# Performance work log

Hardware: AMD Instinct MI355X
Metric: run time of the kernel (lower is better)

## Reference

```python
import jax, jax.numpy as jnp
import numpy as np

B, T, D_IN, D_OUT = 4, 2048, 1024, 1024


def setup_inputs() -> dict:
    key = jax.random.key(0)
    k1, k2, k3, k4 = jax.random.split(key, 4)
    x = jax.random.normal(k1, (B, T, D_IN), dtype=jnp.float32)
    W_q = jax.random.normal(k2, (D_OUT, D_IN), dtype=jnp.float32) * 0.02
    W_k = jax.random.normal(k3, (D_OUT, D_IN), dtype=jnp.float32) * 0.02
    W_v = jax.random.normal(k4, (D_OUT, D_IN), dtype=jnp.float32) * 0.02
    return {"x": x, "W_q": W_q, "W_k": W_k, "W_v": W_v}


def reference(x, W_q, W_k, W_v):
    b, t, d_in = x.shape
    d_out = W_q.shape[0]
    # Linear projections (torch Linear: y = x @ W.T), no bias
    q = jnp.einsum("btd,od->bto", x, W_q)
    k = jnp.einsum("btd,od->bto", x, W_k)
    v = jnp.einsum("btd,od->bto", x, W_v)
    # Raw scores [b, t, t]
    scores = jnp.einsum("bqd,bkd->bqk", q, k)
    # Faithful to the source: tril with diagonal=1 => position i sees j <= i+1
    mask = jnp.tril(jnp.ones((t, t), dtype=bool), k=1)
    scores = jnp.where(mask, scores, -jnp.inf)
    # Scale by sqrt(d_out) (full d_out, single head), stable softmax
    attn = jax.nn.softmax(scores / jnp.sqrt(jnp.asarray(d_out, x.dtype)), axis=-1)
    # dropout=0.0 -> identity
    return jnp.einsum("bqk,bkd->bqd", attn, v)
```

## Files before the change

kernel.cpp:

```cpp
#include <hip/hip_runtime.h>
#include <hip/hip_bf16.h>

typedef unsigned short u16;
typedef __attribute__((ext_vector_type(8))) short short8v;
typedef __attribute__((ext_vector_type(4))) float float4v;

__device__ inline u16 f2b(float f) {
  __hip_bfloat16 h = __float2bfloat16(f);
  union { __hip_bfloat16 h; u16 s; } u;
  u.h = h;
  return u.s;
}

__device__ inline float b2f(u16 s) {
  union { u16 s[2]; float f; } u;
  u.s[0] = 0; u.s[1] = s;
  return u.f;
}

__device__ inline void gload_lds16(const u16* g, u16* l) {
  __builtin_amdgcn_global_load_lds(
      (const __attribute__((address_space(1))) void*)g,
      (__attribute__((address_space(3))) void*)l, 16, 0, 0);
}

__global__ __launch_bounds__(256) void cvt_f32_bf16(const float* __restrict__ in,
                                                    u16* __restrict__ out, int n4) {
  for (int i = blockIdx.x * blockDim.x + threadIdx.x; i < n4;
       i += gridDim.x * blockDim.x) {
    float4 v = ((const float4*)in)[i];
    ushort4 o;
    o.x = f2b(v.x); o.y = f2b(v.y); o.z = f2b(v.z); o.w = f2b(v.w);
    ((ushort4*)out)[i] = o;
  }
}

template <int MODE, typename CT>
__global__ __launch_bounds__(256, 2)
void gemm6(const u16* __restrict__ A, int lda, long sA,
           const u16* __restrict__ B, int ldb, long sB,
           CT* __restrict__ C, int ldc, long sC, int K) {
  constexpr int BM = 128, BN = 128;
  constexpr int A_U16 = BM * 64;
  constexpr int TILE_U16 = (BM + BN) * 64;
  constexpr int TILE_BYTES = TILE_U16 * 2;
  __shared__ __align__(16) u16 lds[2 * TILE_U16];

  const int z = blockIdx.z;
  A += (long)z * sA;
  B += (long)z * sB;

  int bx = blockIdx.x;
  if (MODE == 2) bx = gridDim.x - 1 - bx;
  const int m0 = bx * BM;
  const int n0 = blockIdx.y * BN;
  if (MODE == 1 && n0 > m0 + BM) return;
  int Keff = K;
  if (MODE == 2) Keff = min(m0 + BM + 1, K);
  const int nk = (Keff + 63) >> 6;

  const int tid  = threadIdx.x;
  const int lane = tid & 63;
  const int wid  = tid >> 6;
  const int wr   = wid >> 1;
  const int wc   = wid & 1;

  const u16* gsrc[8];
  int loff[8];
#pragma unroll
  for (int j = 0; j < 4; ++j) {
    int c = tid + j * 256;
    int r = c >> 3;
    int kg = ((c & 7) ^ (r & 7)) * 8;
    gsrc[j] = A + (long)(m0 + r) * lda + kg;
    loff[j] = c * 8;
  }
#pragma unroll
  for (int j = 0; j < 4; ++j) {
    int c = tid + j * 256;
    int r = c >> 3;
    int kg = ((c & 7) ^ (r & 7)) * 8;
    gsrc[4 + j] = B + (long)(n0 + r) * ldb + kg;
    loff[4 + j] = A_U16 + c * 8;
  }

#define STAGE_ALL(T_, DST_)                                                 \
  {                                                                         \
    _Pragma("unroll")                                                       \
    for (int s = 0; s < 8; ++s)                                             \
      gload_lds16(gsrc[s] + (long)(T_) * 64, (DST_) + loff[s]);             \
  }

  const int kl  = (lane >> 4) * 16;
  const int swz = (lane & 7) << 4;
  const int kx0 = kl ^ swz;
  const int kx1 = (64 + kl) ^ swz;
  const int abase = (wr * 64 + (lane & 15)) * 128;
  const int bbase = 2 * A_U16 + (wc * 64 + (lane & 15)) * 128;

  float4v acc[4][4];
#pragma unroll
  for (int i = 0; i < 4; ++i)
#pragma unroll
    for (int j = 0; j < 4; ++j)
      acc[i][j] = (float4v){0.f, 0.f, 0.f, 0.f};

  STAGE_ALL(0, lds);
  asm volatile("s_waitcnt vmcnt(0)" ::: "memory");
  __builtin_amdgcn_s_barrier();

  for (int t = 0; t < nk; ++t) {
    const char* bb = (const char*)lds + (t & 1) * TILE_BYTES;
    u16* sb = lds + ((t & 1) ^ 1) * TILE_U16;

    short8v a0[4], b0[4], a1[4], b1[4];
#pragma unroll
    for (int mi = 0; mi < 4; ++mi) {
      a0[mi] = *(const short8v*)(bb + abase + mi * 2048 + kx0);
      a1[mi] = *(const short8v*)(bb + abase + mi * 2048 + kx1);
    }
#pragma unroll
    for (int ni = 0; ni < 4; ++ni) {
      b0[ni] = *(const short8v*)(bb + bbase + ni * 2048 + kx0);
      b1[ni] = *(const short8v*)(bb + bbase + ni * 2048 + kx1);
    }
    if (t + 1 < nk) STAGE_ALL(t + 1, sb);

    asm volatile("s_waitcnt lgkmcnt(0)" ::: "memory");
    __builtin_amdgcn_sched_barrier(0);
    __builtin_amdgcn_s_setprio(1);
#pragma unroll
    for (int mi = 0; mi < 4; ++mi)
#pragma unroll
      for (int ni = 0; ni < 4; ++ni)
        acc[mi][ni] = __builtin_amdgcn_mfma_f32_16x16x32_bf16(
            a0[mi], b0[ni], acc[mi][ni], 0, 0, 0);
#pragma unroll
    for (int mi = 0; mi < 4; ++mi)
#pragma unroll
      for (int ni = 0; ni < 4; ++ni)
        acc[mi][ni] = __builtin_amdgcn_mfma_f32_16x16x32_bf16(
            a1[mi], b1[ni], acc[mi][ni], 0, 0, 0);
    __builtin_amdgcn_s_setprio(0);

    asm volatile("s_waitcnt vmcnt(0)" ::: "memory");
    __builtin_amdgcn_s_barrier();
  }
#undef STAGE_ALL

  CT* c = C + (long)z * sC;
  const int r0base = m0 + wr * 64 + ((lane >> 4) << 2);
  const int cbase  = n0 + wc * 64 + (lane & 15);
#pragma unroll
  for (int mi = 0; mi < 4; ++mi) {
#pragma unroll
    for (int ni = 0; ni < 4; ++ni) {
      const int r0 = r0base + mi * 16;
      const int cc = cbase + ni * 16;
#pragma unroll
      for (int r = 0; r < 4; ++r) {
        float v = acc[mi][ni][r];
        if constexpr (__is_same(CT, float)) c[(long)(r0 + r) * ldc + cc] = v;
        else                                c[(long)(r0 + r) * ldc + cc] = f2b(v);
      }
    }
  }
}

__global__ __launch_bounds__(256)
void softmax_kernel(u16* __restrict__ SP, int T) {
  const int  i    = blockIdx.x & (T - 1);
  const long base = (long)blockIdx.x * T;
  const int  nvis = min(i + 2, T);
  const int  capJ = min(T, ((i >> 7) << 7) + 192);
  const float scale = 0.03125f;

  __shared__ float red[4];

  const int j0 = threadIdx.x * 8;
  float v[8];
  float m = -INFINITY;
  if (j0 < nvis) {
    short8v raw = *(const short8v*)&SP[base + j0];
#pragma unroll
    for (int e = 0; e < 8; ++e) {
      float f = (j0 + e < nvis) ? b2f((u16)raw[e]) * scale : -INFINITY;
      v[e] = f;
      m = fmaxf(m, f);
    }
  }
#pragma unroll
  for (int o = 32; o; o >>= 1) m = fmaxf(m, __shfl_xor(m, o));
  const int wid = threadIdx.x >> 6;
  if ((threadIdx.x & 63) == 0) red[wid] = m;
  __syncthreads();
  m = fmaxf(fmaxf(red[0], red[1]), fmaxf(red[2], red[3]));
  __syncthreads();

  float s = 0.f;
  if (j0 < nvis) {
#pragma unroll
    for (int e = 0; e < 8; ++e) {
      float p = (j0 + e < nvis) ? __expf(v[e] - m) : 0.f;
      v[e] = p;
      s += p;
    }
  }
#pragma unroll
  for (int o = 32; o; o >>= 1) s += __shfl_xor(s, o);
  if ((threadIdx.x & 63) == 0) red[wid] = s;
  __syncthreads();
  s = red[0] + red[1] + red[2] + red[3];
  const float inv = 1.0f / s;

  if (j0 < capJ) {
    short8v o8;
#pragma unroll
    for (int e = 0; e < 8; ++e)
      o8[e] = (short)f2b((j0 + e < nvis) ? v[e] * inv : 0.f);
    *(short8v*)&SP[base + j0] = o8;
  }
}

extern "C" void kernel_launch(void* const* d_in, const int* in_sizes, int n_in,
                              void* d_out, int out_size, void* d_ws, size_t ws_size,
                              hipStream_t stream) {
  const float* x  = (const float*)d_in[0];
  const float* Wq = (const float*)d_in[1];
  const float* Wk = (const float*)d_in[2];
  const float* Wv = (const float*)d_in[3];
  float* out = (float*)d_out;

  const int B = 4, T = 2048, D = 1024;
  const int M = B * T;
  const long TT = (long)T * T;

  char* ws = (char*)d_ws;
  u16* qk  = (u16*)(ws);
  u16* vt  = (u16*)(ws + (32l << 20));
  u16* xb  = (u16*)(ws + (48l << 20));
  u16* wqk = (u16*)(ws + (64l << 20));
  u16* wv  = (u16*)(ws + (68l << 20));
  u16* S   = (u16*)(ws + (48l << 20));

  cvt_f32_bf16<<<2048, 256, 0, stream>>>(x,  xb,  (M * D) / 4);
  cvt_f32_bf16<<<512,  256, 0, stream>>>(Wq, wqk,               (D * D) / 4);
  cvt_f32_bf16<<<512,  256, 0, stream>>>(Wk, wqk + (long)D * D, (D * D) / 4);
  cvt_f32_bf16<<<512,  256, 0, stream>>>(Wv, wv,  (D * D) / 4);

  gemm6<0, u16><<<dim3(M / 128, 2 * D / 128, 1), 256, 0, stream>>>(
      xb, D, 0, wqk, D, 0, qk, 2 * D, 0, D);
  gemm6<0, u16><<<dim3(D / 128, M / 128, 1), 256, 0, stream>>>(
      wv, D, 0, xb, D, 0, vt, M, 0, D);

  gemm6<1, u16><<<dim3(T / 128, T / 128, B), 256, 0, stream>>>(
      qk, 2 * D, (long)T * 2 * D,
      qk + D, 2 * D, (long)T * 2 * D,
      S, T, TT, D);

  softmax_kernel<<<B * T, 256, 0, stream>>>(S, T);

  gemm6<2, float><<<dim3(T / 128, D / 128, B), 256, 0, stream>>>(
      S, T, TT,
      vt, M, T,
      out, D, (long)T * D, T);
}
```

Before: 168.3 us.

## Use 256x128 GEMM tiles with BK=32 triple-buffered LDS pipeline

```diff
diff --git a/kernel.cpp b/kernel.cpp
--- a/kernel.cpp
+++ b/kernel.cpp
@@ -37,14 +37,14 @@
 
 template <int MODE, typename CT>
 __global__ __launch_bounds__(256, 2)
-void gemm6(const u16* __restrict__ A, int lda, long sA,
+void gemm7(const u16* __restrict__ A, int lda, long sA,
            const u16* __restrict__ B, int ldb, long sB,
            CT* __restrict__ C, int ldc, long sC, int K) {
-  constexpr int BM = 128, BN = 128;
-  constexpr int A_U16 = BM * 64;
-  constexpr int TILE_U16 = (BM + BN) * 64;
-  constexpr int TILE_BYTES = TILE_U16 * 2;
-  __shared__ __align__(16) u16 lds[2 * TILE_U16];
+  constexpr int BM = 256, BN = 128, BK = 32;
+  constexpr int A_U16 = BM * BK;
+  constexpr int BUF_U16 = (BM + BN) * BK;
+  constexpr int BUF_BYTES = BUF_U16 * 2;
+  __shared__ __align__(16) u16 lds[3 * BUF_U16];
 
   const int z = blockIdx.z;
   A += (long)z * sA;
@@ -57,7 +57,7 @@
   if (MODE == 1 && n0 > m0 + BM) return;
   int Keff = K;
   if (MODE == 2) Keff = min(m0 + BM + 1, K);
-  const int nk = (Keff + 63) >> 6;
+  const int nk = (Keff + BK - 1) / BK;
 
   const int tid  = threadIdx.x;
   const int lane = tid & 63;
@@ -65,94 +65,89 @@
   const int wr   = wid >> 1;
   const int wc   = wid & 1;
 
-  const u16* gsrc[8];
-  int loff[8];
+  const u16* gsrc[6];
+  int loff[6];
 #pragma unroll
   for (int j = 0; j < 4; ++j) {
     int c = tid + j * 256;
-    int r = c >> 3;
-    int kg = ((c & 7) ^ (r & 7)) * 8;
+    int L = c >> 3, p = c & 7, l = p ^ (L & 7);
+    int r = 2 * L + (l >> 2), kg = (l & 3) * 8;
     gsrc[j] = A + (long)(m0 + r) * lda + kg;
     loff[j] = c * 8;
   }
 #pragma unroll
-  for (int j = 0; j < 4; ++j) {
+  for (int j = 0; j < 2; ++j) {
     int c = tid + j * 256;
-    int r = c >> 3;
-    int kg = ((c & 7) ^ (r & 7)) * 8;
+    int L = c >> 3, p = c & 7, l = p ^ (L & 7);
+    int r = 2 * L + (l >> 2), kg = (l & 3) * 8;
     gsrc[4 + j] = B + (long)(n0 + r) * ldb + kg;
     loff[4 + j] = A_U16 + c * 8;
   }
 
-#define STAGE_ALL(T_, DST_)                                                 \
+#define STAGE(T_, BUF_)                                                     \
   {                                                                         \
+    u16* base_ = lds + (BUF_) * BUF_U16;                                    \
     _Pragma("unroll")                                                       \
-    for (int s = 0; s < 8; ++s)                                             \
-      gload_lds16(gsrc[s] + (long)(T_) * 64, (DST_) + loff[s]);             \
-  }
-
-  const int kl  = (lane >> 4) * 16;
-  const int swz = (lane & 7) << 4;
-  const int kx0 = kl ^ swz;
-  const int kx1 = (64 + kl) ^ swz;
-  const int abase = (wr * 64 + (lane & 15)) * 128;
-  const int bbase = 2 * A_U16 + (wc * 64 + (lane & 15)) * 128;
-
-  float4v acc[4][4];
-#pragma unroll
-  for (int i = 0; i < 4; ++i)
+    for (int s = 0; s < 6; ++s)                                             \
+      gload_lds16(gsrc[s] + (T_) * BK, base_ + loff[s]);                    \
+  }
+
+  const int g    = lane >> 4;
+  const int rA0  = wr * 128 + (lane & 15);
+  const int rB0  = wc * 64 + (lane & 15);
+  const int lA0  = rA0 >> 1, lB0 = rB0 >> 1;
+  const int cA0  = ((rA0 & 1) << 2) | g;
+  const int cB0  = ((rB0 & 1) << 2) | g;
+  const int offA0 = lA0 * 128 + 16 * (cA0 ^ (lA0 & 7));
+  const int offB0 = 2 * A_U16 + lB0 * 128 + 16 * (cB0 ^ (lB0 & 7));
+
+  float4v acc[8][4];
+#pragma unroll
+  for (int i = 0; i < 8; ++i)
 #pragma unroll
     for (int j = 0; j < 4; ++j)
       acc[i][j] = (float4v){0.f, 0.f, 0.f, 0.f};
 
-  STAGE_ALL(0, lds);
-  asm volatile("s_waitcnt vmcnt(0)" ::: "memory");
-  __builtin_amdgcn_s_barrier();
-
+  STAGE(0, 0);
+  if (nk > 1) STAGE(1, 1);
+
+  int cur = 0;
   for (int t = 0; t < nk; ++t) {
-    const char* bb = (const char*)lds + (t & 1) * TILE_BYTES;
-    u16* sb = lds + ((t & 1) ^ 1) * TILE_U16;
-
-    short8v a0[4], b0[4], a1[4], b1[4];
-#pragma unroll
-    for (int mi = 0; mi < 4; ++mi) {
-      a0[mi] = *(const short8v*)(bb + abase + mi * 2048 + kx0);
-      a1[mi] = *(const short8v*)(bb + abase + mi * 2048 + kx1);
-    }
-#pragma unroll
-    for (int ni = 0; ni < 4; ++ni) {
-      b0[ni] = *(const short8v*)(bb + bbase + ni * 2048 + kx0);
-      b1[ni] = *(const short8v*)(bb + bbase + ni * 2048 + kx1);
-    }
-    if (t + 1 < nk) STAGE_ALL(t + 1, sb);
+    if (t + 1 < nk) asm volatile("s_waitcnt vmcnt(6)" ::: "memory");
+    else            asm volatile("s_waitcnt vmcnt(0)" ::: "memory");
+    __builtin_amdgcn_s_barrier();
+    const char* bb = (const char*)lds + cur * BUF_BYTES;
+    short8v a[8], b[4];
+#pragma unroll
+    for (int mi = 0; mi < 8; ++mi)
+      a[mi] = *(const short8v*)(bb + offA0 + mi * 1024);
+#pragma unroll
+    for (int ni = 0; ni < 4; ++ni)
+      b[ni] = *(const short8v*)(bb + offB0 + ni * 1024);
+
+    const int nxt2 = (cur >= 1) ? cur - 1 : 2;
+    if (t + 2 < nk) STAGE(t + 2, nxt2);
 
     asm volatile("s_waitcnt lgkmcnt(0)" ::: "memory");
     __builtin_amdgcn_sched_barrier(0);
     __builtin_amdgcn_s_setprio(1);
 #pragma unroll
-    for (int mi = 0; mi < 4; ++mi)
+    for (int mi = 0; mi < 8; ++mi)
 #pragma unroll
       for (int ni = 0; ni < 4; ++ni)
         acc[mi][ni] = __builtin_amdgcn_mfma_f32_16x16x32_bf16(
-            a0[mi], b0[ni], acc[mi][ni], 0, 0, 0);
-#pragma unroll
-    for (int mi = 0; mi < 4; ++mi)
-#pragma unroll
-      for (int ni = 0; ni < 4; ++ni)
-        acc[mi][ni] = __builtin_amdgcn_mfma_f32_16x16x32_bf16(
-            a1[mi], b1[ni], acc[mi][ni], 0, 0, 0);
+            a[mi], b[ni], acc[mi][ni], 0, 0, 0);
     __builtin_amdgcn_s_setprio(0);
 
-    asm volatile("s_waitcnt vmcnt(0)" ::: "memory");
-    __builtin_amdgcn_s_barrier();
-  }
-#undef STAGE_ALL
+    cur = (cur < 2) ? cur + 1 : 0;
+  }
+#undef STAGE
 
   CT* c = C + (long)z * sC;
-  const int r0base = m0 + wr * 64 + ((lane >> 4) << 2);
+  const int r0base = m0 + wr * 128 + ((lane >> 4) << 2);
   const int cbase  = n0 + wc * 64 + (lane & 15);
 #pragma unroll
-  for (int mi = 0; mi < 4; ++mi) {
+  for (int mi = 0; mi < 8; ++mi) {
 #pragma unroll
     for (int ni = 0; ni < 4; ++ni) {
       const int r0 = r0base + mi * 16;
@@ -172,7 +167,7 @@
   const int  i    = blockIdx.x & (T - 1);
   const long base = (long)blockIdx.x * T;
   const int  nvis = min(i + 2, T);
-  const int  capJ = min(T, ((i >> 7) << 7) + 192);
+  const int  capJ = min(T, ((i >> 8) << 8) + 288);
   const float scale = 0.03125f;
 
   __shared__ float red[4];
@@ -248,19 +243,19 @@
   cvt_f32_bf16<<<512,  256, 0, stream>>>(Wk, wqk + (long)D * D, (D * D) / 4);
   cvt_f32_bf16<<<512,  256, 0, stream>>>(Wv, wv,  (D * D) / 4);
 
-  gemm6<0, u16><<<dim3(M / 128, 2 * D / 128, 1), 256, 0, stream>>>(
+  gemm7<0, u16><<<dim3(M / 256, 2 * D / 128, 1), 256, 0, stream>>>(
       xb, D, 0, wqk, D, 0, qk, 2 * D, 0, D);
-  gemm6<0, u16><<<dim3(D / 128, M / 128, 1), 256, 0, stream>>>(
+  gemm7<0, u16><<<dim3(D / 256, M / 128, 1), 256, 0, stream>>>(
       wv, D, 0, xb, D, 0, vt, M, 0, D);
 
-  gemm6<1, u16><<<dim3(T / 128, T / 128, B), 256, 0, stream>>>(
+  gemm7<1, u16><<<dim3(T / 256, T / 128, B), 256, 0, stream>>>(
       qk, 2 * D, (long)T * 2 * D,
       qk + D, 2 * D, (long)T * 2 * D,
       S, T, TT, D);
 
   softmax_kernel<<<B * T, 256, 0, stream>>>(S, T);
 
-  gemm6<2, float><<<dim3(T / 128, D / 128, B), 256, 0, stream>>>(
+  gemm7<2, float><<<dim3(T / 256, D / 128, B), 256, 0, stream>>>(
       S, T, TT,
       vt, M, T,
       out, D, (long)T * D, T);
```

After: 176.8 us. 5.0% more time.
